# Kernel optimization log

Hardware: AMD Instinct MI355X
Metric: run time of the kernel (lower is better)

## Reference

```python
import jax, jax.numpy as jnp
import numpy as np


def setup_inputs() -> dict:
    key = jax.random.key(0)
    x = jax.random.normal(key, (32, 32, 64, 512), dtype=jnp.float32)
    return {"x": x}


def reference(x):
    I, J, K, L = x.shape
    ks = jnp.arange(K)

    def step(x, i):
        # x: [I,J,K,L]; orthogonalize vector i against vectors 0..i-1
        xi = x[:, :, i, :]                                  # [I,J,L]
        z1 = jnp.einsum('ijl,ijkl->ijk', xi, x)             # <x_i, x_k>
        z2 = jnp.einsum('ijkl,ijkl->ijk', x, x)             # <x_k, x_k>
        z = jnp.where(ks < i, z1 / z2, 0.0)                 # only k < i (torch slices 0:i)
        proj = jnp.einsum('ijk,ijkl->ijl', z, x)            # [I,J,L]
        # torch uses .detach() on the projection before sub_
        xi_new = xi - jax.lax.stop_gradient(proj)
        return x.at[:, :, i, :].set(xi_new), None

    x, _ = jax.lax.scan(step, x, jnp.arange(1, K))
    # normalize each vector: x * 1/sqrt(<x,x>)
    sq = jnp.einsum('ijkl,ijkl->ijk', x, x)                 # [I,J,K]
    inv = 1.0 / jnp.sqrt(sq)
    return x * inv[..., None]
```

## Files before the change

### kernel.cpp

```cpp
#include <hip/hip_runtime.h>
#include <hip/hip_bf16.h>
#include <cmath>

typedef __attribute__((ext_vector_type(4))) float f32x4;
typedef __attribute__((ext_vector_type(8))) short s16x8;
typedef __attribute__((ext_vector_type(4))) short s16x4;
typedef __attribute__((ext_vector_type(4))) unsigned short u16x4;

static constexpr int NCOL = 512;
static constexpr int NBATCH = 1024;
static constexpr int SLOT = 64 * NCOL;
static constexpr int GOFF = 16384;

__device__ inline unsigned short bf16h(float f) {
  return __builtin_bit_cast(unsigned short, __float2bfloat16(f));
}
__device__ inline float bf16f(unsigned short h) {
  unsigned u = ((unsigned)h) << 16;
  return __builtin_bit_cast(float, u);
}

__device__ inline s16x8 ld8(const unsigned short* p) {
  const s16x4 a = *(const s16x4*)(p);
  const s16x4 b = *(const s16x4*)(p + 4);
  s16x8 r;
  r[0]=a[0]; r[1]=a[1]; r[2]=a[2]; r[3]=a[3];
  r[4]=b[0]; r[5]=b[1]; r[6]=b[2]; r[7]=b[3];
  return r;
}

__global__ __launch_bounds__(256) void gs_gram_kernel(const float* __restrict__ x,
                                                      float* __restrict__ outbuf)
{
  __shared__ unsigned short Hs[64][72];
  __shared__ unsigned short Ls[64][72];

  const int b = blockIdx.x;
  const int t = threadIdx.x;
  const int lane = t & 63;
  const int w = t >> 6;

  const float* __restrict__ X = x + (size_t)b * SLOT;

  f32x4 acc[4];
#pragma unroll
  for (int j = 0; j < 4; ++j) { acc[j][0] = 0.f; acc[j][1] = 0.f; acc[j][2] = 0.f; acc[j][3] = 0.f; }

  const int lrow = t >> 4;
  const int lcol = (t & 15) * 4;
  const int frow = lane & 15;
  const int fk   = (lane >> 4) * 8;

  for (int ch = 0; ch < 8; ++ch) {
    __syncthreads();
#pragma unroll
    for (int p = 0; p < 4; ++p) {
      const int r = lrow + 16 * p;
      const f32x4 v = *(const f32x4*)(X + (size_t)r * NCOL + ch * 64 + lcol);
      u16x4 hv, lv;
#pragma unroll
      for (int j = 0; j < 4; ++j) {
        const unsigned short h = bf16h(v[j]);
        hv[j] = h;
        lv[j] = bf16h(v[j] - bf16f(h));
      }
      *(u16x4*)&Hs[r][lcol] = hv;
      *(u16x4*)&Ls[r][lcol] = lv;
    }
    __syncthreads();
#pragma unroll
    for (int s = 0; s < 2; ++s) {
      const int kc = s * 32 + fk;
      const s16x8 ha = *(const s16x8*)&Hs[16 * w + frow][kc];
      const s16x8 la = *(const s16x8*)&Ls[16 * w + frow][kc];
#pragma unroll
      for (int bt = 0; bt < 4; ++bt) {
        const s16x8 hb = *(const s16x8*)&Hs[16 * bt + frow][kc];
        const s16x8 lb = *(const s16x8*)&Ls[16 * bt + frow][kc];
        acc[bt] = __builtin_amdgcn_mfma_f32_16x16x32_bf16(ha, hb, acc[bt], 0, 0, 0);
        acc[bt] = __builtin_amdgcn_mfma_f32_16x16x32_bf16(ha, lb, acc[bt], 0, 0, 0);
        acc[bt] = __builtin_amdgcn_mfma_f32_16x16x32_bf16(la, hb, acc[bt], 0, 0, 0);
      }
    }
  }

  float* __restrict__ Gs = outbuf + (size_t)b * SLOT + GOFF;
  const int drow = (lane >> 4) * 4;
  const int dcol = lane & 15;
#pragma unroll
  for (int bt = 0; bt < 4; ++bt)
#pragma unroll
    for (int rr = 0; rr < 4; ++rr)
      Gs[(16 * w + drow + rr) * 64 + 16 * bt + dcol] = acc[bt][rr];
}

__global__ __launch_bounds__(64) void gs_solve_kernel(float* __restrict__ outbuf)
{
  __shared__ float Cs[64][68];
  __shared__ float ISN[64];

  const int b = blockIdx.x;
  const int j = threadIdx.x;
  float* __restrict__ slot = outbuf + (size_t)b * SLOT;
  const float* __restrict__ Gs = slot + GOFF;

  float wr[64];
#pragma unroll
  for (int c = 0; c < 16; ++c) {
    const f32x4 v = *(const f32x4*)(Gs + j * 64 + 4 * c);
    wr[4 * c + 0] = v[0]; wr[4 * c + 1] = v[1]; wr[4 * c + 2] = v[2]; wr[4 * c + 3] = v[3];
  }

  {
    const float nk = __shfl(wr[0], 0);
    const float inv = 1.0f / nk;
    Cs[j][0] = wr[0] * inv;
    if (j == 0) ISN[0] = sqrtf(inv);
  }
#pragma unroll
  for (int k = 1; k < 64; ++k) {
    float a0 = 0.f, a1 = 0.f, a2 = 0.f, a3 = 0.f;
    const int K4 = k >> 2;
#pragma unroll
    for (int m4 = 0; m4 < K4; ++m4) {
      const f32x4 c4 = *(const f32x4*)&Cs[k][4 * m4];
      a0 += c4[0] * wr[4 * m4 + 0];
      a1 += c4[1] * wr[4 * m4 + 1];
      a2 += c4[2] * wr[4 * m4 + 2];
      a3 += c4[3] * wr[4 * m4 + 3];
    }
#pragma unroll
    for (int m = 4 * K4; m < k; ++m) a0 += Cs[k][m] * wr[m];
    wr[k] -= (a0 + a1) + (a2 + a3);
    const float nk = __shfl(wr[k], k);
    const float inv = 1.0f / nk;
    Cs[j][k] = wr[k] * inv;
    if (j == 0) ISN[k] = sqrtf(inv);
  }

  float ti[64];
  ti[0] = (j == 0) ? 1.0f : 0.0f;
#pragma unroll
  for (int i = 1; i < 64; ++i) {
    float a0 = 0.f, a1 = 0.f, a2 = 0.f, a3 = 0.f;
    const int I4 = i >> 2;
#pragma unroll
    for (int m4 = 0; m4 < I4; ++m4) {
      const f32x4 c4 = *(const f32x4*)&Cs[i][4 * m4];
      a0 += c4[0] * ti[4 * m4 + 0];
      a1 += c4[1] * ti[4 * m4 + 1];
      a2 += c4[2] * ti[4 * m4 + 2];
      a3 += c4[3] * ti[4 * m4 + 3];
    }
#pragma unroll
    for (int m = 4 * I4; m < i; ++m) a0 += Cs[i][m] * ti[m];
    ti[i] = ((i == j) ? 1.0f : 0.0f) - ((a0 + a1) + (a2 + a3));
  }

  unsigned short* __restrict__ TL = (unsigned short*)&Cs[0][0];
#pragma unroll
  for (int i = 0; i < 64; ++i) {
    const float tf = ISN[i] * ti[i];
    const unsigned short h = bf16h(tf);
    TL[i * 64 + j] = h;
    TL[4096 + i * 64 + j] = bf16h(tf - bf16f(h));
  }
  __syncthreads();
  const unsigned int* __restrict__ TL32 = (const unsigned int*)TL;
  unsigned int* __restrict__ slotT = (unsigned int*)slot;
#pragma unroll
  for (int q = 0; q < 64; ++q) slotT[j + 64 * q] = TL32[j + 64 * q];
}

__global__ __launch_bounds__(256) void gs_apply_kernel(const float* __restrict__ x,
                                                       float* __restrict__ outbuf)
{
  __shared__ unsigned short XTh[64][68];
  __shared__ unsigned short XTl[64][68];

  const int b = blockIdx.x;
  const int t = threadIdx.x;
  const int lane = t & 63;
  const int w = t >> 6;

  float* __restrict__ slot = outbuf + (size_t)b * SLOT;
  const unsigned short* __restrict__ slotU = (const unsigned short*)slot;

  const int frow = lane & 15;
  const int fk = (lane >> 4) * 8;

  s16x8 tah[2], tal[2];
#pragma unroll
  for (int ks = 0; ks < 2; ++ks) {
    tah[ks] = *(const s16x8*)&slotU[(16 * w + frow) * 64 + ks * 32 + fk];
    tal[ks] = *(const s16x8*)&slotU[4096 + (16 * w + frow) * 64 + ks * 32 + fk];
  }
  __syncthreads();

  const float* __restrict__ X = x + (size_t)b * SLOT;
  const int lrow4 = (t >> 4) * 4;
  const int lcol4 = (t & 15) * 4;

  for (int ch = 0; ch < 8; ++ch) {
    if (ch) __syncthreads();
    float vr[4][4];
#pragma unroll
    for (int p = 0; p < 4; ++p) {
      const f32x4 v = *(const f32x4*)(X + (size_t)(lrow4 + p) * NCOL + ch * 64 + lcol4);
      vr[p][0] = v[0]; vr[p][1] = v[1]; vr[p][2] = v[2]; vr[p][3] = v[3];
    }
#pragma unroll
    for (int jj = 0; jj < 4; ++jj) {
      u16x4 hv, lv;
#pragma unroll
      for (int p = 0; p < 4; ++p) {
        const unsigned short h = bf16h(vr[p][jj]);
        hv[p] = h;
        lv[p] = bf16h(vr[p][jj] - bf16f(h));
      }
      *(u16x4*)&XTh[lcol4 + jj][lrow4] = hv;
      *(u16x4*)&XTl[lcol4 + jj][lrow4] = lv;
    }
    __syncthreads();

    f32x4 oacc[4];
#pragma unroll
    for (int q = 0; q < 4; ++q) { oacc[q][0] = 0.f; oacc[q][1] = 0.f; oacc[q][2] = 0.f; oacc[q][3] = 0.f; }

#pragma unroll
    for (int ks = 0; ks < 2; ++ks) {
      const int kc = ks * 32 + fk;
#pragma unroll
      for (int ct = 0; ct < 4; ++ct) {
        const s16x8 xbh = ld8(&XTh[ct * 16 + frow][kc]);
        const s16x8 xbl = ld8(&XTl[ct * 16 + frow][kc]);
        oacc[ct] = __builtin_amdgcn_mfma_f32_16x16x32_bf16(tah[ks], xbh, oacc[ct], 0, 0, 0);
        oacc[ct] = __builtin_amdgcn_mfma_f32_16x16x32_bf16(tah[ks], xbl, oacc[ct], 0, 0, 0);
        oacc[ct] = __builtin_amdgcn_mfma_f32_16x16x32_bf16(tal[ks], xbh, oacc[ct], 0, 0, 0);
      }
    }

    const int drow = (lane >> 4) * 4;
    const int dcol = lane & 15;
#pragma unroll
    for (int ct = 0; ct < 4; ++ct)
#pragma unroll
      for (int rr = 0; rr < 4; ++rr)
        slot[(size_t)(16 * w + drow + rr) * NCOL + ch * 64 + ct * 16 + dcol] = oacc[ct][rr];
  }
}

extern "C" void kernel_launch(void* const* d_in, const int* in_sizes, int n_in,
                              void* d_out, int out_size, void* d_ws, size_t ws_size,
                              hipStream_t stream) {
  const float* x = (const float*)d_in[0];
  float* out = (float*)d_out;
  gs_gram_kernel<<<NBATCH, 256, 0, stream>>>(x, out);
  gs_solve_kernel<<<NBATCH, 64, 0, stream>>>(out);
  gs_apply_kernel<<<NBATCH, 256, 0, stream>>>(x, out);
}
```

Before: 103.9 us.

## Fuse Gram computation and triangular solve into one kernel via LDS

```diff
diff --git a/kernel.cpp b/kernel.cpp
--- a/kernel.cpp
+++ b/kernel.cpp
@@ -10,7 +10,6 @@
 static constexpr int NCOL = 512;
 static constexpr int NBATCH = 1024;
 static constexpr int SLOT = 64 * NCOL;
-static constexpr int GOFF = 16384;
 
 __device__ inline unsigned short bf16h(float f) {
   return __builtin_bit_cast(unsigned short, __float2bfloat16(f));
@@ -29,11 +28,16 @@
   return r;
 }
 
-__global__ __launch_bounds__(256) void gs_gram_kernel(const float* __restrict__ x,
-                                                      float* __restrict__ outbuf)
+union GramLds {
+  struct { unsigned short Hs[64][72]; unsigned short Ls[64][72]; } s;
+  float GW[64][68];
+};
+
+__global__ __launch_bounds__(256, 4) void gs_gram_solve_kernel(const float* __restrict__ x,
+                                                               float* __restrict__ outbuf)
 {
-  __shared__ unsigned short Hs[64][72];
-  __shared__ unsigned short Ls[64][72];
+  __shared__ GramLds U;
+  __shared__ float ISN[64];
 
   const int b = blockIdx.x;
   const int t = threadIdx.x;
@@ -44,7 +48,7 @@
 
   f32x4 acc[4];
 #pragma unroll
-  for (int j = 0; j < 4; ++j) { acc[j][0] = 0.f; acc[j][1] = 0.f; acc[j][2] = 0.f; acc[j][3] = 0.f; }
+  for (int q = 0; q < 4; ++q) { acc[q][0] = 0.f; acc[q][1] = 0.f; acc[q][2] = 0.f; acc[q][3] = 0.f; }
 
   const int lrow = t >> 4;
   const int lcol = (t & 15) * 4;
@@ -64,57 +68,52 @@
         hv[j] = h;
         lv[j] = bf16h(v[j] - bf16f(h));
       }
-      *(u16x4*)&Hs[r][lcol] = hv;
-      *(u16x4*)&Ls[r][lcol] = lv;
+      *(u16x4*)&U.s.Hs[r][lcol] = hv;
+      *(u16x4*)&U.s.Ls[r][lcol] = lv;
     }
     __syncthreads();
 #pragma unroll
     for (int s = 0; s < 2; ++s) {
       const int kc = s * 32 + fk;
-      const s16x8 ha = *(const s16x8*)&Hs[16 * w + frow][kc];
-      const s16x8 la = *(const s16x8*)&Ls[16 * w + frow][kc];
+      const s16x8 ha = *(const s16x8*)&U.s.Hs[16 * w + frow][kc];
+      const s16x8 la = *(const s16x8*)&U.s.Ls[16 * w + frow][kc];
 #pragma unroll
       for (int bt = 0; bt < 4; ++bt) {
-        const s16x8 hb = *(const s16x8*)&Hs[16 * bt + frow][kc];
-        const s16x8 lb = *(const s16x8*)&Ls[16 * bt + frow][kc];
+        const s16x8 hb = *(const s16x8*)&U.s.Hs[16 * bt + frow][kc];
+        const s16x8 lb = *(const s16x8*)&U.s.Ls[16 * bt + frow][kc];
         acc[bt] = __builtin_amdgcn_mfma_f32_16x16x32_bf16(ha, hb, acc[bt], 0, 0, 0);
         acc[bt] = __builtin_amdgcn_mfma_f32_16x16x32_bf16(ha, lb, acc[bt], 0, 0, 0);
         acc[bt] = __builtin_amdgcn_mfma_f32_16x16x32_bf16(la, hb, acc[bt], 0, 0, 0);
       }
     }
   }
-
-  float* __restrict__ Gs = outbuf + (size_t)b * SLOT + GOFF;
-  const int drow = (lane >> 4) * 4;
-  const int dcol = lane & 15;
-#pragma unroll
-  for (int bt = 0; bt < 4; ++bt)
-#pragma unroll
-    for (int rr = 0; rr < 4; ++rr)
-      Gs[(16 * w + drow + rr) * 64 + 16 * bt + dcol] = acc[bt][rr];
-}
-
-__global__ __launch_bounds__(64) void gs_solve_kernel(float* __restrict__ outbuf)
-{
-  __shared__ float Cs[64][68];
-  __shared__ float ISN[64];
-
-  const int b = blockIdx.x;
-  const int j = threadIdx.x;
-  float* __restrict__ slot = outbuf + (size_t)b * SLOT;
-  const float* __restrict__ Gs = slot + GOFF;
+  __syncthreads();
+
+  {
+    const int drow = (lane >> 4) * 4;
+    const int dcol = lane & 15;
+#pragma unroll
+    for (int bt = 0; bt < 4; ++bt)
+#pragma unroll
+      for (int rr = 0; rr < 4; ++rr)
+        U.GW[16 * w + drow + rr][16 * bt + dcol] = acc[bt][rr];
+  }
+  __syncthreads();
+
+  if (t >= 64) return;
+  const int j = t;
 
   float wr[64];
 #pragma unroll
   for (int c = 0; c < 16; ++c) {
-    const f32x4 v = *(const f32x4*)(Gs + j * 64 + 4 * c);
+    const f32x4 v = *(const f32x4*)&U.GW[j][4 * c];
     wr[4 * c + 0] = v[0]; wr[4 * c + 1] = v[1]; wr[4 * c + 2] = v[2]; wr[4 * c + 3] = v[3];
   }
 
   {
     const float nk = __shfl(wr[0], 0);
     const float inv = 1.0f / nk;
-    Cs[j][0] = wr[0] * inv;
+    U.GW[j][0] = wr[0] * inv;
     if (j == 0) ISN[0] = sqrtf(inv);
   }
 #pragma unroll
@@ -123,18 +122,18 @@
     const int K4 = k >> 2;
 #pragma unroll
     for (int m4 = 0; m4 < K4; ++m4) {
-      const f32x4 c4 = *(const f32x4*)&Cs[k][4 * m4];
+      const f32x4 c4 = *(const f32x4*)&U.GW[k][4 * m4];
       a0 += c4[0] * wr[4 * m4 + 0];
       a1 += c4[1] * wr[4 * m4 + 1];
       a2 += c4[2] * wr[4 * m4 + 2];
       a3 += c4[3] * wr[4 * m4 + 3];
     }
 #pragma unroll
-    for (int m = 4 * K4; m < k; ++m) a0 += Cs[k][m] * wr[m];
+    for (int m = 4 * K4; m < k; ++m) a0 += U.GW[k][m] * wr[m];
     wr[k] -= (a0 + a1) + (a2 + a3);
     const float nk = __shfl(wr[k], k);
     const float inv = 1.0f / nk;
-    Cs[j][k] = wr[k] * inv;
+    U.GW[j][k] = wr[k] * inv;
     if (j == 0) ISN[k] = sqrtf(inv);
   }
 
@@ -146,18 +145,18 @@
     const int I4 = i >> 2;
 #pragma unroll
     for (int m4 = 0; m4 < I4; ++m4) {
-      const f32x4 c4 = *(const f32x4*)&Cs[i][4 * m4];
+      const f32x4 c4 = *(const f32x4*)&U.GW[i][4 * m4];
       a0 += c4[0] * ti[4 * m4 + 0];
       a1 += c4[1] * ti[4 * m4 + 1];
       a2 += c4[2] * ti[4 * m4 + 2];
       a3 += c4[3] * ti[4 * m4 + 3];
     }
 #pragma unroll
-    for (int m = 4 * I4; m < i; ++m) a0 += Cs[i][m] * ti[m];
+    for (int m = 4 * I4; m < i; ++m) a0 += U.GW[i][m] * ti[m];
     ti[i] = ((i == j) ? 1.0f : 0.0f) - ((a0 + a1) + (a2 + a3));
   }
 
-  unsigned short* __restrict__ TL = (unsigned short*)&Cs[0][0];
+  unsigned short* __restrict__ TL = (unsigned short*)&U.GW[0][0];
 #pragma unroll
   for (int i = 0; i < 64; ++i) {
     const float tf = ISN[i] * ti[i];
@@ -165,7 +164,7 @@
     TL[i * 64 + j] = h;
     TL[4096 + i * 64 + j] = bf16h(tf - bf16f(h));
   }
-  __syncthreads();
+  float* __restrict__ slot = outbuf + (size_t)b * SLOT;
   const unsigned int* __restrict__ TL32 = (const unsigned int*)TL;
   unsigned int* __restrict__ slotT = (unsigned int*)slot;
 #pragma unroll
@@ -255,7 +254,6 @@
                               hipStream_t stream) {
   const float* x = (const float*)d_in[0];
   float* out = (float*)d_out;
-  gs_gram_kernel<<<NBATCH, 256, 0, stream>>>(x, out);
-  gs_solve_kernel<<<NBATCH, 64, 0, stream>>>(out);
+  gs_gram_solve_kernel<<<NBATCH, 256, 0, stream>>>(x, out);
   gs_apply_kernel<<<NBATCH, 256, 0, stream>>>(x, out);
 }
```

New measurement: 178.2 us. 71.4% more time.
